# Performance work log

Measured on AMD Instinct MI355X. Metric: run time of the kernel, lower is better.

Reference implementation:

```python
import jax, jax.numpy as jnp
import numpy as np

B, L, H, D_IN = 64, 4096, 128, 3

def setup_inputs() -> dict:
    key = jax.random.key(0)
    ks = jax.random.split(key, 9)
    def lin_w(k, fan_in, shape):
        bound = 1.0 / np.sqrt(fan_in)
        return jax.random.uniform(k, shape, jnp.float32, -bound, bound)
    return {
        "x": jax.random.normal(ks[0], (B, L, D_IN), jnp.float32),
        "Wp": lin_w(ks[1], D_IN, (D_IN, H)), "bp": lin_w(ks[2], D_IN, (H,)),
        "Wz": lin_w(ks[3], H, (H, H)),      "bz": lin_w(ks[4], H, (H,)),
        "Wh": lin_w(ks[5], H, (H, H)),      "bh": lin_w(ks[6], H, (H,)),
        "Wg": lin_w(ks[7], H, (H, 1)),      "bg": lin_w(ks[8], H, (1,)),
    }

def reference(x, Wp, bp, Wz, bz, Wh, bh, Wg, bg):
    # Batched projections across all timesteps (B, L, H)
    inp = x @ Wp + bp                      # input_proj
    z = jax.nn.sigmoid(inp @ Wz + bz)      # update gate
    h_tilde = jnp.tanh(inp @ Wh + bh)      # candidate
    # Linear recurrence h_t = a_t * h_{t-1} + b_t, h_{-1} = 0
    a = 1.0 - z
    b = z * h_tilde
    def combine(c1, c2):
        a1, b1 = c1
        a2, b2 = c2
        return (a1 * a2, b1 * a2 + b2)
    _, h = jax.lax.associative_scan(combine, (a, b), axis=1)  # h_t (since h_{-1}=0)
    # Readout uses h BEFORE the update at each step: preds_t = gauss_head(h_{t-1})
    h_prev = jnp.concatenate([jnp.zeros_like(h[:, :1]), h[:, :-1]], axis=1)
    preds = h_prev @ Wg + bg               # (B, L, 1)
    return preds
```

## Files before the change

### kernel.cpp

```cpp
#include <hip/hip_runtime.h>
#include <hip/hip_bf16.h>
#include <stdint.h>

#define B_   64
#define L_   4096
#define H_   128
#define T_   64
#define C_   (L_/T_)
#define BH_  (B_*H_)
#define PADI 136

typedef __attribute__((ext_vector_type(8))) short short8;
typedef __attribute__((ext_vector_type(4))) short short4v;
typedef __attribute__((ext_vector_type(4))) float floatx4;

#define LOG2E 1.44269504088896340736f

__device__ __forceinline__ unsigned short f2bf(float f){
    unsigned int u = __float_as_uint(f);
    u += 0x7FFFu + ((u >> 16) & 1u);
    return (unsigned short)(u >> 16);
}
__device__ __forceinline__ float bf2f(unsigned short s){
    return __uint_as_float(((unsigned int)s) << 16);
}

__global__ void prep_w(const float* __restrict__ Wz, const float* __restrict__ Wh,
                       unsigned short* __restrict__ WzT, unsigned short* __restrict__ WhT){
    int b = blockIdx.x;
    const float* W = (b < 16) ? Wz : Wh;
    unsigned short* WT = (b < 16) ? WzT : WhT;
    int b16 = b & 15, tid = threadIdx.x;
    #pragma unroll
    for (int it = 0; it < 4; ++it){
        int idx = b16*1024 + it*256 + tid;
        int n = idx >> 7, k = idx & 127;
        WT[idx] = f2bf(W[k*H_ + n]);
    }
}

__global__ __launch_bounds__(256, 4)
void carry_scan(const float* __restrict__ aggA, const float* __restrict__ aggH,
                float* __restrict__ carry){
    int idx = blockIdx.x*256 + threadIdx.x;
    float c = 0.0f;
    #pragma unroll
    for (int cc = 0; cc < C_; ++cc){
        carry[cc*BH_ + idx] = c;
        c = fmaf(aggA[cc*BH_ + idx], c, aggH[cc*BH_ + idx]);
    }
}


__global__ __launch_bounds__(256, 4)
void gates_agg(const float* __restrict__ x,
               const float* __restrict__ Wp, const float* __restrict__ bp,
               const float* __restrict__ bz, const float* __restrict__ bh,
               const float* __restrict__ Wg,
               const unsigned short* __restrict__ WzT,
               const unsigned short* __restrict__ WhT,
               float* __restrict__ aggA, float* __restrict__ aggH,
               float* __restrict__ sloc, unsigned short* __restrict__ pw_g)
{
    __shared__ __align__(16) unsigned short s_ab[H_*H_];
    __shared__ float s_bz[H_], s_bh[H_], s_wg[H_];
    __shared__ float s_part[256];
    unsigned short* inp_lds = s_ab;

    const int bid = blockIdx.x;
    const int bb  = bid / C_;
    const int cc  = bid % C_;
    const int t0g = cc * T_;
    const int tid = threadIdx.x;
    const int wv = tid >> 6, lane = tid & 63, quad = lane >> 4, l15 = lane & 15;

    if (tid < H_){ s_bz[tid] = bz[tid]; s_bh[tid] = bh[tid]; s_wg[tid] = Wg[tid]; }

    {
        const int h0 = (tid & 15) * 8;
        float w0[8], w1[8], w2[8], b0[8];
        #pragma unroll
        for (int m = 0; m < 8; ++m){
            w0[m] = Wp[h0+m]; w1[m] = Wp[H_+h0+m]; w2[m] = Wp[2*H_+h0+m];
            b0[m] = bp[h0+m];
        }
        #pragma unroll
        for (int it = 0; it < 4; ++it){
            int t = (tid >> 4) + it*16;
            const float* xr = x + ((size_t)bb*L_ + t0g + t)*3;
            float x0 = xr[0], x1 = xr[1], x2 = xr[2];
            short8 pk;
            #pragma unroll
            for (int m = 0; m < 8; ++m){
                float v = b0[m];
                v = fmaf(x0, w0[m], v);
                v = fmaf(x1, w1[m], v);
                v = fmaf(x2, w2[m], v);
                pk[m] = (short)f2bf(v);
            }
            *(short8*)&inp_lds[t*PADI + h0] = pk;
        }
    }
    __syncthreads();

    const int ct0 = wv*2;

    floatx4 accz[4][2];
    #pragma unroll
    for (int r = 0; r < 4; ++r)
        #pragma unroll
        for (int c = 0; c < 2; ++c) accz[r][c] = (floatx4){0.f,0.f,0.f,0.f};
    #pragma unroll
    for (int kk = 0; kk < 4; ++kk){
        short8 af[4], bfr[2];
        #pragma unroll
        for (int r = 0; r < 4; ++r)
            af[r] = *(const short8*)&inp_lds[(r*16 + l15)*PADI + kk*32 + quad*8];
        #pragma unroll
        for (int c = 0; c < 2; ++c)
            bfr[c] = *(const short8*)&WzT[((ct0+c)*16 + l15)*H_ + kk*32 + quad*8];
        #pragma unroll
        for (int r = 0; r < 4; ++r)
            #pragma unroll
            for (int c = 0; c < 2; ++c)
                accz[r][c] = __builtin_amdgcn_mfma_f32_16x16x32_bf16(af[r], bfr[c], accz[r][c], 0, 0, 0);
    }

    floatx4 acch[4][2];
    #pragma unroll
    for (int r = 0; r < 4; ++r)
        #pragma unroll
        for (int c = 0; c < 2; ++c) acch[r][c] = (floatx4){0.f,0.f,0.f,0.f};
    #pragma unroll
    for (int kk = 0; kk < 4; ++kk){
        short8 af[4], bfr[2];
        #pragma unroll
        for (int r = 0; r < 4; ++r)
            af[r] = *(const short8*)&inp_lds[(r*16 + l15)*PADI + kk*32 + quad*8];
        #pragma unroll
        for (int c = 0; c < 2; ++c)
            bfr[c] = *(const short8*)&WhT[((ct0+c)*16 + l15)*H_ + kk*32 + quad*8];
        #pragma unroll
        for (int r = 0; r < 4; ++r)
            #pragma unroll
            for (int c = 0; c < 2; ++c)
                acch[r][c] = __builtin_amdgcn_mfma_f32_16x16x32_bf16(af[r], bfr[c], acch[r][c], 0, 0, 0);
    }
    __syncthreads();

    #pragma unroll
    for (int r = 0; r < 4; ++r){
        #pragma unroll
        for (int c = 0; c < 2; ++c){
            int col = (ct0+c)*16 + l15;
            float vbz = s_bz[col], vbh = s_bh[col];
            short8 pk;
            #pragma unroll
            for (int e = 0; e < 4; ++e){
                float szb = accz[r][c][e] + vbz;
                float a = __builtin_amdgcn_rcpf(1.0f + __builtin_amdgcn_exp2f(szb * LOG2E));
                unsigned short abf = f2bf(a);
                float af_ = bf2f(abf);
                float z = 1.0f - af_;
                float shb = acch[r][c][e] + vbh;
                float e2 = __builtin_amdgcn_exp2f(2.0f*LOG2E*fabsf(shb));
                float tt = 1.0f - 2.0f*__builtin_amdgcn_rcpf(e2 + 1.0f);
                float bt = z * copysignf(tt, shb);
                pk[2*e]   = (short)abf;
                pk[2*e+1] = (short)f2bf(bt);
            }
            int ch = (r*4 + quad) ^ l15;
            *(short8*)&s_ab[col*H_ + ch*8] = pk;
        }
    }
    __syncthreads();

    if (tid < H_){
        float A = 1.0f, h = 0.0f;
        float wgv = s_wg[tid];
        #pragma unroll
        for (int t4 = 0; t4 < 16; ++t4){
            int base = tid*H_ + ((t4 ^ (tid & 15)) << 3);
            short8 pr = *(const short8*)&s_ab[base];
            short8 wb;
            #pragma unroll
            for (int e = 0; e < 4; ++e){
                float aa = bf2f((unsigned short)pr[2*e]);
                float bv = bf2f((unsigned short)pr[2*e+1]);
                wb[2*e]   = (short)f2bf(h * wgv);
                wb[2*e+1] = (short)f2bf(A * wgv);
                A *= aa;
                h = fmaf(aa, h, bv);
            }
            *(short8*)&s_ab[base] = wb;
        }
        aggA[cc*BH_ + bb*H_ + tid] = A;
        aggH[cc*BH_ + bb*H_ + tid] = h;
    }
    __syncthreads();

    {
        unsigned short* dst = pw_g + (size_t)bid*(T_*H_);
        #pragma unroll
        for (int i = 0; i < 8; ++i){
            int idx = i*256 + tid;
            int col = idx >> 4, t4 = idx & 15;
            short8 pr = *(const short8*)&s_ab[col*H_ + ((t4 ^ (col & 15)) << 3)];
            short4v pw4;
            pw4[0] = pr[1]; pw4[1] = pr[3]; pw4[2] = pr[5]; pw4[3] = pr[7];
            *(short4v*)&dst[col*T_ + t4*4] = pw4;
        }
    }

    {
        int t = tid & 63, w4 = tid >> 6;
        int t4 = t >> 2, e2 = (t & 3)*2;
        float s = 0.0f;
        #pragma unroll
        for (int j = 0; j < 32; ++j){
            int col = w4*32 + j;
            s += bf2f(s_ab[col*H_ + ((t4 ^ (col & 15)) << 3) + e2]);
        }
        s_part[w4*64 + t] = s;
    }
    __syncthreads();
    if (tid < 64)
        sloc[(size_t)bid*T_ + tid] =
            s_part[tid] + s_part[64+tid] + s_part[128+tid] + s_part[192+tid];
}

__global__ __launch_bounds__(256, 4)
void apply2(const unsigned short* __restrict__ pw_g,
            const float* __restrict__ carry,
            const float* __restrict__ sloc, const float* __restrict__ bg,
            float* __restrict__ preds)
{
    __shared__ float s_c[H_];
    __shared__ float s_part[256];
    const int bid = blockIdx.x;
    const int bb  = bid / C_;
    const int cc  = bid % C_;
    const int t0g = cc * T_;
    const int tid = threadIdx.x;

    if (tid < H_) s_c[tid] = carry[cc*BH_ + bb*H_ + tid];
    __syncthreads();

    {
        const unsigned short* src = pw_g + (size_t)bid*(T_*H_);
        int t = tid & 63, w4 = tid >> 6;
        float s = 0.0f;
        #pragma unroll
        for (int j = 0; j < 32; ++j){
            int col = w4*32 + j;
            s += s_c[col] * bf2f(src[col*T_ + t]);
        }
        s_part[w4*64 + t] = s;
    }
    __syncthreads();
    if (tid < 64){
        float s = s_part[tid] + s_part[64+tid] + s_part[128+tid] + s_part[192+tid];
        preds[(size_t)bb*L_ + t0g + tid] = s + sloc[(size_t)bid*T_ + tid] + bg[0];
    }
}

extern "C" void kernel_launch(void* const* d_in, const int* in_sizes, int n_in,
                              void* d_out, int out_size, void* d_ws, size_t ws_size,
                              hipStream_t stream){
    const float* x  = (const float*)d_in[0];
    const float* Wp = (const float*)d_in[1];
    const float* bp = (const float*)d_in[2];
    const float* Wz = (const float*)d_in[3];
    const float* bz = (const float*)d_in[4];
    const float* Wh = (const float*)d_in[5];
    const float* bh = (const float*)d_in[6];
    const float* Wg = (const float*)d_in[7];
    const float* bg = (const float*)d_in[8];
    float* preds = (float*)d_out;

    uint8_t* w8 = (uint8_t*)d_ws;
    unsigned short* WzT = (unsigned short*)(w8);
    unsigned short* WhT = (unsigned short*)(w8 + 32768);
    float* aggA  = (float*)(w8 + 65536);
    float* aggH  = (float*)(w8 + 65536 + 4u*BH_*C_);
    float* sloc  = (float*)(w8 + 65536 + 8u*BH_*C_);
    float* carry = (float*)(w8 + 65536 + 12u*BH_*C_);
    unsigned short* pw_g = (unsigned short*)(w8 + 65536 + 16u*BH_*C_);

    hipLaunchKernelGGL(prep_w, dim3(32), dim3(256), 0, stream, Wz, Wh, WzT, WhT);
    hipLaunchKernelGGL(gates_agg, dim3(B_*C_), dim3(256), 0, stream,
                       x, Wp, bp, bz, bh, Wg, WzT, WhT, aggA, aggH, sloc, pw_g);
    hipLaunchKernelGGL(carry_scan, dim3(BH_/256), dim3(256), 0, stream,
                       aggA, aggH, carry);
    hipLaunchKernelGGL(apply2, dim3(B_*C_), dim3(256), 0, stream,
                       pw_g, carry, sloc, bg, preds);
}
```

Before: 173.2 us.

## Replace serial chunk carry scan with wave-level Kogge-Stone scan and vectorize apply

```diff
diff --git a/kernel.cpp b/kernel.cpp
--- a/kernel.cpp
+++ b/kernel.cpp
@@ -13,6 +13,7 @@
 typedef __attribute__((ext_vector_type(8))) short short8;
 typedef __attribute__((ext_vector_type(4))) short short4v;
 typedef __attribute__((ext_vector_type(4))) float floatx4;
+typedef __attribute__((ext_vector_type(2))) float floatx2;
 
 #define LOG2E 1.44269504088896340736f
 
@@ -40,15 +41,21 @@
 }
 
 __global__ __launch_bounds__(256, 4)
-void carry_scan(const float* __restrict__ aggA, const float* __restrict__ aggH,
-                float* __restrict__ carry){
-    int idx = blockIdx.x*256 + threadIdx.x;
-    float c = 0.0f;
-    #pragma unroll
-    for (int cc = 0; cc < C_; ++cc){
-        carry[cc*BH_ + idx] = c;
-        c = fmaf(aggA[cc*BH_ + idx], c, aggH[cc*BH_ + idx]);
-    }
+void carry_kogge(const floatx2* __restrict__ agg2, float* __restrict__ carry_g){
+    const int row  = blockIdx.x*4 + (threadIdx.x >> 6);
+    const int lane = threadIdx.x & 63;
+    floatx2 v = agg2[(size_t)row*C_ + lane];
+    #pragma unroll
+    for (int d = 1; d < 64; d <<= 1){
+        float oA = __shfl_up(v[0], d, 64);
+        float oH = __shfl_up(v[1], d, 64);
+        if (lane >= d){
+            v[1] = fmaf(oH, v[0], v[1]);
+            v[0] = oA * v[0];
+        }
+    }
+    float eh = __shfl_up(v[1], 1, 64);
+    carry_g[(size_t)row*C_ + lane] = (lane == 0) ? 0.0f : eh;
 }
 
 
@@ -59,7 +66,7 @@
                const float* __restrict__ Wg,
                const unsigned short* __restrict__ WzT,
                const unsigned short* __restrict__ WhT,
-               float* __restrict__ aggA, float* __restrict__ aggH,
+               floatx2* __restrict__ agg2,
                float* __restrict__ sloc, unsigned short* __restrict__ pw_g)
 {
     __shared__ __align__(16) unsigned short s_ab[H_*H_];
@@ -194,8 +201,7 @@
             }
             *(short8*)&s_ab[base] = wb;
         }
-        aggA[cc*BH_ + bb*H_ + tid] = A;
-        aggH[cc*BH_ + bb*H_ + tid] = h;
+        agg2[(size_t)(bb*H_ + tid)*C_ + cc] = (floatx2){A, h};
     }
     __syncthreads();
 
@@ -231,7 +237,7 @@
 
 __global__ __launch_bounds__(256, 4)
 void apply2(const unsigned short* __restrict__ pw_g,
-            const float* __restrict__ carry,
+            const float* __restrict__ carry_g,
             const float* __restrict__ sloc, const float* __restrict__ bg,
             float* __restrict__ preds)
 {
@@ -242,20 +248,36 @@
     const int cc  = bid % C_;
     const int t0g = cc * T_;
     const int tid = threadIdx.x;
-
-    if (tid < H_) s_c[tid] = carry[cc*BH_ + bb*H_ + tid];
+    const int wv = tid >> 6, lane = tid & 63;
+
+    if (tid < H_) s_c[tid] = carry_g[(size_t)(bb*H_ + tid)*C_ + cc];
     __syncthreads();
 
     {
         const unsigned short* src = pw_g + (size_t)bid*(T_*H_);
-        int t = tid & 63, w4 = tid >> 6;
-        float s = 0.0f;
-        #pragma unroll
-        for (int j = 0; j < 32; ++j){
-            int col = w4*32 + j;
-            s += s_c[col] * bf2f(src[col*T_ + t]);
-        }
-        s_part[w4*64 + t] = s;
+        const int cl = lane >> 3, t8 = lane & 7;
+        float s8[8];
+        #pragma unroll
+        for (int e = 0; e < 8; ++e) s8[e] = 0.0f;
+        #pragma unroll
+        for (int g = 0; g < 4; ++g){
+            int col = wv*32 + g*8 + cl;
+            short8 pw8 = *(const short8*)&src[col*T_ + t8*8];
+            float cv = s_c[col];
+            #pragma unroll
+            for (int e = 0; e < 8; ++e)
+                s8[e] = fmaf(cv, bf2f((unsigned short)pw8[e]), s8[e]);
+        }
+        #pragma unroll
+        for (int d = 8; d < 64; d <<= 1)
+            #pragma unroll
+            for (int e = 0; e < 8; ++e)
+                s8[e] += __shfl_xor(s8[e], d, 64);
+        if (lane < 8){
+            #pragma unroll
+            for (int e = 0; e < 8; ++e)
+                s_part[wv*64 + t8*8 + e] = s8[e];
+        }
     }
     __syncthreads();
     if (tid < 64){
@@ -281,17 +303,15 @@
     uint8_t* w8 = (uint8_t*)d_ws;
     unsigned short* WzT = (unsigned short*)(w8);
     unsigned short* WhT = (unsigned short*)(w8 + 32768);
-    float* aggA  = (float*)(w8 + 65536);
-    float* aggH  = (float*)(w8 + 65536 + 4u*BH_*C_);
-    float* sloc  = (float*)(w8 + 65536 + 8u*BH_*C_);
-    float* carry = (float*)(w8 + 65536 + 12u*BH_*C_);
+    floatx2* agg2 = (floatx2*)(w8 + 65536);
+    float* sloc   = (float*)(w8 + 65536 + 8u*BH_*C_);
+    float* carry  = (float*)(w8 + 65536 + 12u*BH_*C_);
     unsigned short* pw_g = (unsigned short*)(w8 + 65536 + 16u*BH_*C_);
 
     hipLaunchKernelGGL(prep_w, dim3(32), dim3(256), 0, stream, Wz, Wh, WzT, WhT);
     hipLaunchKernelGGL(gates_agg, dim3(B_*C_), dim3(256), 0, stream,
-                       x, Wp, bp, bz, bh, Wg, WzT, WhT, aggA, aggH, sloc, pw_g);
-    hipLaunchKernelGGL(carry_scan, dim3(BH_/256), dim3(256), 0, stream,
-                       aggA, aggH, carry);
+                       x, Wp, bp, bz, bh, Wg, WzT, WhT, agg2, sloc, pw_g);
+    hipLaunchKernelGGL(carry_kogge, dim3(BH_/4), dim3(256), 0, stream, agg2, carry);
     hipLaunchKernelGGL(apply2, dim3(B_*C_), dim3(256), 0, stream,
                        pw_g, carry, sloc, bg, preds);
 }
```

After: 157.0 us. 1.1x faster.
